# Kernel optimization log

Measured on AMD Instinct MI355X. Metric: run time of the kernel, lower is better.

Reference implementation:

```python
import jax, jax.numpy as jnp
import numpy as np

B, IN, V, H, OUT = 4096, 1024, 48, 512, 64

def setup_inputs() -> dict:
    key = jax.random.key(0)
    ks = jax.random.split(key, 6)
    s = 0.02
    x = jax.random.normal(ks[0], (B, IN), dtype=jnp.float32)
    # stacked per-vocab MLP params: hidden layers have bias, last layer bias=False
    W1 = jax.random.normal(ks[1], (V, IN, H), dtype=jnp.float32) * s
    b1 = jax.random.normal(ks[2], (V, H), dtype=jnp.float32) * s
    W2 = jax.random.normal(ks[3], (V, H, H), dtype=jnp.float32) * s
    b2 = jax.random.normal(ks[4], (V, H), dtype=jnp.float32) * s
    W3 = jax.random.normal(ks[5], (V, H, OUT), dtype=jnp.float32) * s
    return {"x": x, "W1": W1, "b1": b1, "W2": W2, "b2": b2, "W3": W3}

def reference(x, W1, b1, W2, b2, W3):
    # grouped GEMM over the vocab axis; equivalent to the per-MLP loop + cat
    h = jax.nn.relu(jnp.einsum('bi,vih->bvh', x, W1) + b1)      # [B, V, H]
    h = jax.nn.relu(jnp.einsum('bvh,vhk->bvk', h, W2) + b2)     # [B, V, H]
    o = jnp.einsum('bvk,vko->bvo', h, W3)                        # [B, V, OUT]
    # torch.cat([...], dim=-1) == reshape since outputs are in vocab order
    return o.reshape(x.shape[0], V * OUT)
```

## Files before the change

kernel.cpp:

```cpp
#include <hip/hip_runtime.h>

#define B_SZ   4096
#define IN_SZ  1024
#define V_SZ   48
#define H_SZ   512
#define OUT_SZ 64

typedef __attribute__((ext_vector_type(4))) float f32x4;
typedef __attribute__((ext_vector_type(8))) short bf16x8;
typedef __attribute__((ext_vector_type(4))) short short4v;
typedef __attribute__((ext_vector_type(4))) float float4v;

__device__ __forceinline__ short f2bf(float f){
    unsigned u = __builtin_bit_cast(unsigned, f);
    u += 0x7fffu + ((u >> 16) & 1u);
    return (short)(u >> 16);
}

__device__ __forceinline__ void gl2lds16(const void* g, void* l){
    __builtin_amdgcn_global_load_lds(
        (const __attribute__((address_space(1))) void*)g,
        (__attribute__((address_space(3))) void*)l, 16, 0, 0);
}

__global__ void k_convert_x(const float* __restrict__ x, short* __restrict__ xb){
    int i = blockIdx.x * 256 + threadIdx.x;
    float4v f = ((const float4v*)x)[i];
    short4v o = { f2bf(f.x), f2bf(f.y), f2bf(f.z), f2bf(f.w) };
    ((short4v*)xb)[i] = o;
}

__global__ __launch_bounds__(256) void k_transpose_cvt4(
    const float* __restrict__ in, short* __restrict__ out, int R, int C)
{
    __shared__ short t[64][68];
    int v  = blockIdx.z;
    int c0 = blockIdx.x * 64, r0 = blockIdx.y * 64;
    int tid = threadIdx.x;
    size_t base = (size_t)v * R * C;
    const float* inp = in + base + (size_t)r0 * C + c0;
    int g    = tid >> 4;
    int col4 = (tid & 15) * 4;
    #pragma unroll
    for (int p = 0; p < 4; ++p){
        int row = p*16 + g;
        float4v f = *(const float4v*)&inp[(size_t)row * C + col4];
        short4v s = { f2bf(f.x), f2bf(f.y), f2bf(f.z), f2bf(f.w) };
        *(short4v*)&t[row][col4] = s;
    }
    __syncthreads();
    short* outp = out + base + (size_t)c0 * R + r0;
    int r4 = (tid & 15) * 4;
    #pragma unroll
    for (int p = 0; p < 4; ++p){
        int c = p*16 + g;
        short4v s = { t[r4+0][c], t[r4+1][c], t[r4+2][c], t[r4+3][c] };
        *(short4v*)&outp[(size_t)c * R + r4] = s;
    }
}

__global__ __launch_bounds__(256) void k_gemm1(
    const short* __restrict__ xb, const short* __restrict__ W1t,
    const float* __restrict__ b1, short* __restrict__ h1)
{
    __shared__ __align__(16) short As[128*64];
    __shared__ __align__(16) short Bs[128*64];
    const int tid  = threadIdx.x;
    const int lane = tid & 63, wave = tid >> 6;
    const int l15  = lane & 15, quad = lane >> 4;
    const int wm = wave & 1, wn = wave >> 1;
    const int M0 = blockIdx.x * 128;
    const int N0 = blockIdx.y * 128;
    const int v  = blockIdx.z;

    const short* a_base = xb  + (size_t)M0 * IN_SZ;
    const short* b_base = W1t + ((size_t)v * H_SZ + N0) * IN_SZ;

    const short* asrc[4]; const short* bsrc[4]; short* adst[4]; short* bdst[4];
    #pragma unroll
    for (int j = 0; j < 4; ++j){
        int p   = j*256 + tid;
        int row = p >> 3;
        int w   = (p & 7) ^ (row & 7);
        asrc[j] = a_base + (size_t)row * IN_SZ + w*8;
        bsrc[j] = b_base + (size_t)row * IN_SZ + w*8;
        adst[j] = &As[(size_t)(j*256 + (tid & ~63)) * 8];
        bdst[j] = &Bs[(size_t)(j*256 + (tid & ~63)) * 8];
    }

    f32x4 acc[4][4];
    #pragma unroll
    for (int i = 0; i < 4; ++i)
        #pragma unroll
        for (int j = 0; j < 4; ++j) acc[i][j] = (f32x4){0.f,0.f,0.f,0.f};

    for (int k0 = 0; k0 < IN_SZ; k0 += 64){
        #pragma unroll
        for (int j = 0; j < 4; ++j){
            gl2lds16(asrc[j] + k0, adst[j]);
            gl2lds16(bsrc[j] + k0, bdst[j]);
        }
        __syncthreads();
        #pragma unroll
        for (int kk = 0; kk < 2; ++kk){
            bf16x8 a[4], b[4];
            #pragma unroll
            for (int tm = 0; tm < 4; ++tm){
                int m = wm*64 + tm*16 + l15;
                int slot = m*8 + ((kk*4 + quad) ^ (m & 7));
                a[tm] = *(const bf16x8*)&As[slot*8];
            }
            #pragma unroll
            for (int tn = 0; tn < 4; ++tn){
                int n = wn*64 + tn*16 + l15;
                int slot = n*8 + ((kk*4 + quad) ^ (n & 7));
                b[tn] = *(const bf16x8*)&Bs[slot*8];
            }
            #pragma unroll
            for (int tm = 0; tm < 4; ++tm)
                #pragma unroll
                for (int tn = 0; tn < 4; ++tn)
                    acc[tm][tn] = __builtin_amdgcn_mfma_f32_16x16x32_bf16(
                        a[tm], b[tn], acc[tm][tn], 0, 0, 0);
        }
        __syncthreads();
    }

    const float* bv = b1 + (size_t)v * H_SZ;
    short* cv = h1 + (size_t)v * (B_SZ*H_SZ);
    #pragma unroll
    for (int tn = 0; tn < 4; ++tn){
        int col = N0 + wn*64 + tn*16 + l15;
        float bb = bv[col];
        #pragma unroll
        for (int tm = 0; tm < 4; ++tm){
            int rowb = M0 + wm*64 + tm*16 + quad*4;
            #pragma unroll
            for (int r = 0; r < 4; ++r){
                float val = acc[tm][tn][r] + bb;
                val = val > 0.f ? val : 0.f;
                cv[(size_t)(rowb + r) * H_SZ + col] = f2bf(val);
            }
        }
    }
}

__global__ __launch_bounds__(512) void k_gemm23(
    const short* __restrict__ h, const short* __restrict__ W2t,
    const float* __restrict__ b2, const short* __restrict__ W3t,
    float* __restrict__ out)
{
    __shared__ __align__(16) short As[64*64];
    __shared__ __align__(16) short Bs[512*64];
    const int tid  = threadIdx.x;
    const int lane = tid & 63, wave = tid >> 6;
    const int l15  = lane & 15, quad = lane >> 4;
    const int M0 = blockIdx.x * 64;
    const int v  = blockIdx.y;

    const short* hv  = h   + (size_t)v * (B_SZ*H_SZ) + (size_t)M0 * H_SZ;
    const short* w2v = W2t + (size_t)v * (H_SZ*H_SZ);
    const short* w3v = W3t + (size_t)v * (OUT_SZ*H_SZ);

    const int rowT = tid >> 3;
    const int wT   = (tid & 7) ^ (rowT & 7);
    const short* asrc  = hv  + (size_t)rowT * H_SZ + wT*8;
    const short* bsrc0 = w2v + (size_t)rowT * H_SZ + wT*8;
    short* adst  = &As[(size_t)(tid & ~63) * 8];
    short* bdst0 = &Bs[(size_t)(tid & ~63) * 8];

    f32x4 acc[4][4];
    #pragma unroll
    for (int i = 0; i < 4; ++i)
        #pragma unroll
        for (int j = 0; j < 4; ++j) acc[i][j] = (f32x4){0.f,0.f,0.f,0.f};

    for (int k0 = 0; k0 < H_SZ; k0 += 64){
        gl2lds16(asrc + k0, adst);
        #pragma unroll
        for (int j = 0; j < 8; ++j)
            gl2lds16(bsrc0 + (size_t)j*(64*H_SZ) + k0, bdst0 + (size_t)j*512*8);
        __syncthreads();
        #pragma unroll
        for (int kk = 0; kk < 2; ++kk){
            bf16x8 a[4], b[4];
            #pragma unroll
            for (int tm = 0; tm < 4; ++tm){
                int m = tm*16 + l15;
                int slot = m*8 + ((kk*4 + quad) ^ (m & 7));
                a[tm] = *(const bf16x8*)&As[slot*8];
            }
            #pragma unroll
            for (int tn = 0; tn < 4; ++tn){
                int n = wave*64 + tn*16 + l15;
                int slot = n*8 + ((kk*4 + quad) ^ (n & 7));
                b[tn] = *(const bf16x8*)&Bs[slot*8];
            }
            #pragma unroll
            for (int tm = 0; tm < 4; ++tm)
                #pragma unroll
                for (int tn = 0; tn < 4; ++tn)
                    acc[tm][tn] = __builtin_amdgcn_mfma_f32_16x16x32_bf16(
                        a[tm], b[tn], acc[tm][tn], 0, 0, 0);
        }
        __syncthreads();
    }

    const float* bv = b2 + (size_t)v * H_SZ;
    #pragma unroll
    for (int tn = 0; tn < 4; ++tn){
        int col = wave*64 + tn*16 + l15;
        float bb = bv[col];
        int u = col >> 3, c7 = col & 7;
        #pragma unroll
        for (int tm = 0; tm < 4; ++tm){
            int rowb = tm*16 + quad*4;
            #pragma unroll
            for (int r = 0; r < 4; ++r){
                int row = rowb + r;
                float val = acc[tm][tn][r] + bb;
                val = val > 0.f ? val : 0.f;
                Bs[row*512 + ((u ^ (row & 7))*8) + c7] = f2bf(val);
            }
        }
    }
    __syncthreads();

    if (wave < 4){
        f32x4 acc3[4];
        #pragma unroll
        for (int i = 0; i < 4; ++i) acc3[i] = (f32x4){0.f,0.f,0.f,0.f};
        const int n3 = wave*16 + l15;
        const short* b3p = &w3v[(size_t)n3 * H_SZ + quad*8];
        #pragma unroll
        for (int kk = 0; kk < 16; ++kk){
            bf16x8 bfrag = *(const bf16x8*)&b3p[kk*32];
            int u = kk*4 + quad;
            #pragma unroll
            for (int tm = 0; tm < 4; ++tm){
                int m = tm*16 + l15;
                bf16x8 afrag = *(const bf16x8*)&Bs[m*512 + ((u ^ (m & 7))*8)];
                acc3[tm] = __builtin_amdgcn_mfma_f32_16x16x32_bf16(
                    afrag, bfrag, acc3[tm], 0, 0, 0);
            }
        }
        const int col = v*OUT_SZ + wave*16 + l15;
        #pragma unroll
        for (int tm = 0; tm < 4; ++tm){
            int rowb = M0 + tm*16 + quad*4;
            #pragma unroll
            for (int r = 0; r < 4; ++r)
                out[(size_t)(rowb + r) * (V_SZ*OUT_SZ) + col] = acc3[tm][r];
        }
    }
}

extern "C" void kernel_launch(void* const* d_in, const int* in_sizes, int n_in,
                              void* d_out, int out_size, void* d_ws, size_t ws_size,
                              hipStream_t stream)
{
    (void)in_sizes; (void)n_in; (void)out_size; (void)ws_size;
    const float* x  = (const float*)d_in[0];
    const float* W1 = (const float*)d_in[1];
    const float* b1 = (const float*)d_in[2];
    const float* W2 = (const float*)d_in[3];
    const float* b2 = (const float*)d_in[4];
    const float* W3 = (const float*)d_in[5];
    float* out = (float*)d_out;

    char* ws = (char*)d_ws;
    short* xb  = (short*)ws;  ws += (size_t)B_SZ * IN_SZ * 2;
    short* W1t = (short*)ws;  ws += (size_t)V_SZ * H_SZ * IN_SZ * 2;
    short* W2t = (short*)ws;  ws += (size_t)V_SZ * H_SZ * H_SZ * 2;
    short* W3t = (short*)ws;  ws += (size_t)V_SZ * OUT_SZ * H_SZ * 2;
    short* h1  = (short*)ws;

    k_convert_x<<<dim3(B_SZ*IN_SZ/1024), dim3(256), 0, stream>>>(x, xb);
    k_transpose_cvt4<<<dim3(H_SZ/64,  IN_SZ/64, V_SZ), dim3(256), 0, stream>>>(W1, W1t, IN_SZ, H_SZ);
    k_transpose_cvt4<<<dim3(H_SZ/64,  H_SZ/64,  V_SZ), dim3(256), 0, stream>>>(W2, W2t, H_SZ, H_SZ);
    k_transpose_cvt4<<<dim3(OUT_SZ/64,H_SZ/64,  V_SZ), dim3(256), 0, stream>>>(W3, W3t, H_SZ, OUT_SZ);

    k_gemm1 <<<dim3(B_SZ/128, H_SZ/128, V_SZ), dim3(256), 0, stream>>>(xb, W1t, b1, h1);
    k_gemm23<<<dim3(B_SZ/64, V_SZ), dim3(512), 0, stream>>>(h1, W2t, b2, W3t, out);
}
```

Baseline: 653.9 us.

## Remap GEMM grids to XCD-aware 1D order and split GEMM3 across all waves

Both GEMM kernels switch to a flattened 1D grid whose block index is decoded so that blocks landing on the same XCD (round-robin by index mod 8) share the same vocab weights and, in gemm1, the same N tile pair. The aim is better L2 reuse of W1/W2 slices within each XCD's private cache. In addition, the final W3 GEMM in gemm23 now uses all 8 waves (each handling half the rows) instead of 4, which removes idle waves in that phase. The mapping hardcodes the grid shape and assumes round-robin dispatch across 8 XCDs.

```diff
diff --git a/kernel.cpp b/kernel.cpp
--- a/kernel.cpp
+++ b/kernel.cpp
@@ -69,9 +69,15 @@
     const int lane = tid & 63, wave = tid >> 6;
     const int l15  = lane & 15, quad = lane >> 4;
     const int wm = wave & 1, wn = wave >> 1;
-    const int M0 = blockIdx.x * 128;
-    const int N0 = blockIdx.y * 128;
-    const int v  = blockIdx.z;
+
+    const int f    = blockIdx.x;
+    const int xcd  = f & 7, slot = f >> 3;
+    const int pair = slot >> 5;
+    const int mi   = slot & 31;
+    const int p    = xcd * 24 + pair;
+    const int v    = p >> 2;
+    const int N0   = (p & 3) * 128;
+    const int M0   = mi * 128;
 
     const short* a_base = xb  + (size_t)M0 * IN_SZ;
     const short* b_base = W1t + ((size_t)v * H_SZ + N0) * IN_SZ;
@@ -79,9 +85,9 @@
     const short* asrc[4]; const short* bsrc[4]; short* adst[4]; short* bdst[4];
     #pragma unroll
     for (int j = 0; j < 4; ++j){
-        int p   = j*256 + tid;
-        int row = p >> 3;
-        int w   = (p & 7) ^ (row & 7);
+        int pp  = j*256 + tid;
+        int row = pp >> 3;
+        int w   = (pp & 7) ^ (row & 7);
         asrc[j] = a_base + (size_t)row * IN_SZ + w*8;
         bsrc[j] = b_base + (size_t)row * IN_SZ + w*8;
         adst[j] = &As[(size_t)(j*256 + (tid & ~63)) * 8];
@@ -107,14 +113,14 @@
             #pragma unroll
             for (int tm = 0; tm < 4; ++tm){
                 int m = wm*64 + tm*16 + l15;
-                int slot = m*8 + ((kk*4 + quad) ^ (m & 7));
-                a[tm] = *(const bf16x8*)&As[slot*8];
+                int sl = m*8 + ((kk*4 + quad) ^ (m & 7));
+                a[tm] = *(const bf16x8*)&As[sl*8];
             }
             #pragma unroll
             for (int tn = 0; tn < 4; ++tn){
                 int n = wn*64 + tn*16 + l15;
-                int slot = n*8 + ((kk*4 + quad) ^ (n & 7));
-                b[tn] = *(const bf16x8*)&Bs[slot*8];
+                int sl = n*8 + ((kk*4 + quad) ^ (n & 7));
+                b[tn] = *(const bf16x8*)&Bs[sl*8];
             }
             #pragma unroll
             for (int tm = 0; tm < 4; ++tm)
@@ -155,8 +161,13 @@
     const int tid  = threadIdx.x;
     const int lane = tid & 63, wave = tid >> 6;
     const int l15  = lane & 15, quad = lane >> 4;
-    const int M0 = blockIdx.x * 64;
-    const int v  = blockIdx.y;
+
+    const int f    = blockIdx.x;
+    const int xcd  = f & 7, slot = f >> 3;
+    const int vloc = slot >> 6;
+    const int mi   = slot & 63;
+    const int v    = xcd * 6 + vloc;
+    const int M0   = mi * 64;
 
     const short* hv  = h   + (size_t)v * (B_SZ*H_SZ) + (size_t)M0 * H_SZ;
     const short* w2v = W2t + (size_t)v * (H_SZ*H_SZ);
@@ -187,14 +198,14 @@
             #pragma unroll
             for (int tm = 0; tm < 4; ++tm){
                 int m = tm*16 + l15;
-                int slot = m*8 + ((kk*4 + quad) ^ (m & 7));
-                a[tm] = *(const bf16x8*)&As[slot*8];
+                int sl = m*8 + ((kk*4 + quad) ^ (m & 7));
+                a[tm] = *(const bf16x8*)&As[sl*8];
             }
             #pragma unroll
             for (int tn = 0; tn < 4; ++tn){
                 int n = wave*64 + tn*16 + l15;
-                int slot = n*8 + ((kk*4 + quad) ^ (n & 7));
-                b[tn] = *(const bf16x8*)&Bs[slot*8];
+                int sl = n*8 + ((kk*4 + quad) ^ (n & 7));
+                b[tn] = *(const bf16x8*)&Bs[sl*8];
             }
             #pragma unroll
             for (int tm = 0; tm < 4; ++tm)
@@ -226,28 +237,29 @@
     }
     __syncthreads();
 
-    if (wave < 4){
-        f32x4 acc3[4];
-        #pragma unroll
-        for (int i = 0; i < 4; ++i) acc3[i] = (f32x4){0.f,0.f,0.f,0.f};
-        const int n3 = wave*16 + l15;
+    {
+        const int mh = wave >> 2, nq = wave & 3;
+        f32x4 acc3[2];
+        #pragma unroll
+        for (int i = 0; i < 2; ++i) acc3[i] = (f32x4){0.f,0.f,0.f,0.f};
+        const int n3 = nq*16 + l15;
         const short* b3p = &w3v[(size_t)n3 * H_SZ + quad*8];
         #pragma unroll
         for (int kk = 0; kk < 16; ++kk){
             bf16x8 bfrag = *(const bf16x8*)&b3p[kk*32];
             int u = kk*4 + quad;
             #pragma unroll
-            for (int tm = 0; tm < 4; ++tm){
-                int m = tm*16 + l15;
+            for (int tm = 0; tm < 2; ++tm){
+                int m = mh*32 + tm*16 + l15;
                 bf16x8 afrag = *(const bf16x8*)&Bs[m*512 + ((u ^ (m & 7))*8)];
                 acc3[tm] = __builtin_amdgcn_mfma_f32_16x16x32_bf16(
                     afrag, bfrag, acc3[tm], 0, 0, 0);
             }
         }
-        const int col = v*OUT_SZ + wave*16 + l15;
-        #pragma unroll
-        for (int tm = 0; tm < 4; ++tm){
-            int rowb = M0 + tm*16 + quad*4;
+        const int col = v*OUT_SZ + nq*16 + l15;
+        #pragma unroll
+        for (int tm = 0; tm < 2; ++tm){
+            int rowb = M0 + mh*32 + tm*16 + quad*4;
             #pragma unroll
             for (int r = 0; r < 4; ++r)
                 out[(size_t)(rowb + r) * (V_SZ*OUT_SZ) + col] = acc3[tm][r];
@@ -280,6 +292,6 @@
     k_transpose_cvt4<<<dim3(H_SZ/64,  H_SZ/64,  V_SZ), dim3(256), 0, stream>>>(W2, W2t, H_SZ, H_SZ);
     k_transpose_cvt4<<<dim3(OUT_SZ/64,H_SZ/64,  V_SZ), dim3(256), 0, stream>>>(W3, W3t, H_SZ, OUT_SZ);
 
-    k_gemm1 <<<dim3(B_SZ/128, H_SZ/128, V_SZ), dim3(256), 0, stream>>>(xb, W1t, b1, h1);
-    k_gemm23<<<dim3(B_SZ/64, V_SZ), dim3(512), 0, stream>>>(h1, W2t, b2, W3t, out);
-}
+    k_gemm1 <<<dim3((B_SZ/128)*(H_SZ/128)*V_SZ), dim3(256), 0, stream>>>(xb, W1t, b1, h1);
+    k_gemm23<<<dim3((B_SZ/64)*V_SZ), dim3(512), 0, stream>>>(h1, W2t, b2, W3t, out);
+}
```

Measured after the change: 693.1 us. 1.06x slower.
